# Kernel optimization log

Measured on AMD Instinct MI355X. Metric: run time of the kernel, lower is better.

The kernel has to match this reference:

```python
import jax, jax.numpy as jnp
import numpy as np

B, S, D = 8, 512, 512
H, DK = 64, 8          # 64 heads hardcoded in SelfAttentiveLBLBiLM
WIDTH = 16             # local window width
NL = 2                 # highway layers
N = S + 2 * WIDTH      # padded sequence length


def setup_inputs() -> dict:
    key = jax.random.key(0)
    ks = jax.random.split(key, 12)
    s = 0.02
    return {
        "inputs": jax.random.normal(ks[0], (B, S, D), jnp.float32),
        "left_pad": jax.random.normal(ks[1], (WIDTH, D), jnp.float32) * s,
        "right_pad": jax.random.normal(ks[2], (WIDTH, D), jnp.float32) * s,
        "l_Wqkv": jax.random.normal(ks[3], (3, D, D), jnp.float32) * s,
        "l_bqkv": jnp.zeros((3, D), jnp.float32),
        "l_Wo": jax.random.normal(ks[4], (D, D), jnp.float32) * s,
        "l_bo": jnp.zeros((D,), jnp.float32),
        "r_Wqkv": jax.random.normal(ks[5], (3, D, D), jnp.float32) * s,
        "r_bqkv": jnp.zeros((3, D), jnp.float32),
        "r_Wo": jax.random.normal(ks[6], (D, D), jnp.float32) * s,
        "r_bo": jnp.zeros((D,), jnp.float32),
        "lhw_W": jax.random.normal(ks[7], (NL, 2 * D, D), jnp.float32) * s,
        "lhw_b": jnp.zeros((NL, 2 * D), jnp.float32),
        "rhw_W": jax.random.normal(ks[8], (NL, 2 * D, D), jnp.float32) * s,
        "rhw_b": jnp.zeros((NL, 2 * D), jnp.float32),
    }


def _masks(n, width):
    i = jnp.arange(n)[:, None]
    j = jnp.arange(n)[None, :]
    # local_mask: triu(k=-width-1) * (1 - triu(k=1)) -> i-width-1 <= j <= i
    left = (j <= i) & (j >= i - width - 1)
    # right mask is the full flip of the left mask
    right = (j >= i) & (j <= i + width + 1)
    return left, right


def _mha(x, Wqkv, bqkv, Wo, bo, mask):
    b, n, d = x.shape
    # torch Linear: y = x @ W.T + b, W is [out, in]
    qkv = jnp.einsum("bnd,tod->tbno", x, Wqkv) + bqkv[:, None, None, :]
    q, k, v = [t.reshape(b, n, H, DK).transpose(0, 2, 1, 3) for t in qkv]
    scores = jnp.einsum("bhqd,bhkd->bhqk", q, k) / jnp.sqrt(jnp.float32(DK))
    scores = jnp.where(mask[None, None], scores, jnp.float32(-1e9))
    p = jax.nn.softmax(scores, axis=-1)
    out = jnp.einsum("bhqk,bhkd->bhqd", p, v)
    out = out.transpose(0, 2, 1, 3).reshape(b, n, d)
    return out @ Wo.T + bo


def _highway(x, Ws, bs):
    for l in range(NL):
        proj = x @ Ws[l].T + bs[l]
        nonlin = jax.nn.relu(proj[..., :D])
        gate = jax.nn.sigmoid(proj[..., D:])
        x = gate * x + (1.0 - gate) * nonlin
    return x


def reference(inputs, left_pad, right_pad, l_Wqkv, l_bqkv, l_Wo, l_bo,
              r_Wqkv, r_bqkv, r_Wo, r_bo, lhw_W, lhw_b, rhw_W, rhw_b):
    b = inputs.shape[0]
    new_inputs = jnp.concatenate(
        [jnp.broadcast_to(left_pad[None], (b, WIDTH, D)), inputs,
         jnp.broadcast_to(right_pad[None], (b, WIDTH, D))], axis=1)  # [B, N, D]
    left_mask, right_mask = _masks(N, WIDTH)
    new_left = _mha(new_inputs, l_Wqkv, l_bqkv, l_Wo, l_bo, left_mask)
    new_right = _mha(new_inputs, r_Wqkv, r_bqkv, r_Wo, r_bo, right_mask)
    # per-step loop indexes position start + width -> slice [WIDTH : WIDTH + S]
    left_out = _highway(new_left[:, WIDTH:WIDTH + S], lhw_W, lhw_b)
    right_out = _highway(new_right[:, WIDTH:WIDTH + S], rhw_W, rhw_b)
    last = jnp.concatenate([left_out, right_out], axis=-1)  # [B, S, 2D]
    all_layers = last[None]  # [1, B, S, 2D] (single layer stacked on dim 0)
    return (all_layers, last)
```

## Files before the change

### kernel.cpp

```cpp
#include <hip/hip_runtime.h>
#include <math.h>

#define B_ 8
#define S_ 512
#define D_ 512
#define WIDTH_ 16
#define NSEQ 544
#define MROWS 4352
#define MOUT 4096
#define OUTHALF 4194304

typedef _Float16 half8 __attribute__((ext_vector_type(8)));
typedef _Float16 half4 __attribute__((ext_vector_type(4)));
typedef float floatx4 __attribute__((ext_vector_type(4)));

#define GLD16(g, l) __builtin_amdgcn_global_load_lds(                          \
    (const __attribute__((address_space(1))) void*)(g),                        \
    (__attribute__((address_space(3))) void*)(l), 16, 0, 0)

__device__ __forceinline__ float sigmoidf_(float x) {
    return 1.f / (1.f + __expf(-x));
}

__global__ __launch_bounds__(256)
void gemm_qkv(const _Float16* __restrict__ A,
              const _Float16* __restrict__ B0, const _Float16* __restrict__ B1,
              const float* __restrict__ bias0, const float* __restrict__ bias1,
              _Float16* __restrict__ C16) {
    const int lda = 512, ldb = 512, ldc = 1536, K = 512;
    __shared__ _Float16 As[128 * 32];
    __shared__ _Float16 Bs[128 * 32];
    const int t    = threadIdx.x;
    const int wave = t >> 6;
    const int lane = t & 63;
    const int bm = blockIdx.y * 128;
    const int bn = blockIdx.x * 128;
    const int z  = blockIdx.z;
    const _Float16* B = z ? B1 : B0;
    const float* bias = z ? bias1 : bias0;
    _Float16* C = C16 + (size_t)z * MROWS * 1536;
    const int wm = (wave & 1) * 64;
    const int wn = (wave >> 1) * 64;

    const int inst = wave * 2;
    const int r0 = inst * 16 + (lane >> 2);
    const int kf = (lane & 3) * 8;

    const _Float16* Ag0 = A + (size_t)(bm + r0) * lda + kf;
    const _Float16* Ag1 = Ag0 + (size_t)16 * lda;
    const _Float16* Bg0 = B + (size_t)(bn + r0) * ldb + kf;
    const _Float16* Bg1 = Bg0 + (size_t)16 * ldb;
    _Float16* As0 = &As[inst * 512];
    _Float16* As1 = As0 + 512;
    _Float16* Bs0 = &Bs[inst * 512];
    _Float16* Bs1 = Bs0 + 512;

    const int fr = lane & 15;
    const int fq = (lane >> 4) * 8;

    floatx4 acc[4][4] = {};

    for (int k0 = 0; k0 < K; k0 += 32) {
        GLD16(Ag0, As0); GLD16(Ag1, As1);
        GLD16(Bg0, Bs0); GLD16(Bg1, Bs1);
        Ag0 += 32; Ag1 += 32; Bg0 += 32; Bg1 += 32;
        __syncthreads();
        half8 af[4], bf[4];
#pragma unroll
        for (int s = 0; s < 4; s++) {
            af[s] = *(const half8*)&As[(wm + s * 16 + fr) * 32 + fq];
            bf[s] = *(const half8*)&Bs[(wn + s * 16 + fr) * 32 + fq];
        }
#pragma unroll
        for (int i = 0; i < 4; i++)
#pragma unroll
            for (int j = 0; j < 4; j++)
                acc[i][j] = __builtin_amdgcn_mfma_f32_16x16x32_f16(
                    af[i], bf[j], acc[i][j], 0, 0, 0);
        __syncthreads();
    }

    const int rq = (lane >> 4) * 4;
    const int cc = lane & 15;
#pragma unroll
    for (int i = 0; i < 4; i++) {
        const int rbase = bm + wm + i * 16 + rq;
#pragma unroll
        for (int j = 0; j < 4; j++) {
            const int col = bn + wn + j * 16 + cc;
            const float bv = bias[col];
#pragma unroll
            for (int r = 0; r < 4; r++)
                C[(size_t)(rbase + r) * ldc + col] = (_Float16)(acc[i][j][r] + bv);
        }
    }
}

__global__ __launch_bounds__(256)
void gemm_wo(const _Float16* __restrict__ Aall,
             const _Float16* __restrict__ B0, const _Float16* __restrict__ B1,
             const float* __restrict__ bias0, const float* __restrict__ bias1,
             float* __restrict__ xbase,
             _Float16* __restrict__ x16base) {
    const int lda = 512, ldb = 512, K = 512;
    __shared__ _Float16 As[64 * 32];
    __shared__ _Float16 Bs[128 * 32];
    const int t    = threadIdx.x;
    const int wave = t >> 6;
    const int lane = t & 63;
    const int bm = blockIdx.y * 64;
    const int bn = blockIdx.x * 128;
    const int z  = blockIdx.z;
    const _Float16* A = Aall + (size_t)z * MROWS * 512;
    const _Float16* B = z ? B1 : B0;
    const float* bias = z ? bias1 : bias0;
    float* xcol = xbase + z * 512;
    _Float16* x16 = x16base + (size_t)z * MOUT * 512;

    const int wm = (wave & 1) * 32;
    const int wn = (wave >> 1) * 64;

    const int rA = wave * 16 + (lane >> 2);
    const int rB = wave * 32 + (lane >> 2);
    const int kf = (lane & 3) * 8;

    const _Float16* Ag0 = A + (size_t)(bm + rA) * lda + kf;
    const _Float16* Bg0 = B + (size_t)(bn + rB) * ldb + kf;
    const _Float16* Bg1 = Bg0 + (size_t)16 * ldb;
    _Float16* As0 = &As[wave * 512];
    _Float16* Bs0 = &Bs[wave * 1024];
    _Float16* Bs1 = Bs0 + 512;

    const int fr = lane & 15;
    const int fq = (lane >> 4) * 8;

    floatx4 acc[2][4] = {};

    for (int k0 = 0; k0 < K; k0 += 32) {
        GLD16(Ag0, As0);
        GLD16(Bg0, Bs0); GLD16(Bg1, Bs1);
        Ag0 += 32; Bg0 += 32; Bg1 += 32;
        __syncthreads();
        half8 af[2], bf[4];
#pragma unroll
        for (int s = 0; s < 2; s++)
            af[s] = *(const half8*)&As[(wm + s * 16 + fr) * 32 + fq];
#pragma unroll
        for (int s = 0; s < 4; s++)
            bf[s] = *(const half8*)&Bs[(wn + s * 16 + fr) * 32 + fq];
#pragma unroll
        for (int i = 0; i < 2; i++)
#pragma unroll
            for (int j = 0; j < 4; j++)
                acc[i][j] = __builtin_amdgcn_mfma_f32_16x16x32_f16(
                    af[i], bf[j], acc[i][j], 0, 0, 0);
        __syncthreads();
    }

    const int rq = (lane >> 4) * 4;
    const int cc = lane & 15;
#pragma unroll
    for (int i = 0; i < 2; i++) {
        const int rbase = bm + wm + i * 16 + rq;
#pragma unroll
        for (int r = 0; r < 4; r++) {
            const int row = rbase + r;
            const int b = row / NSEQ;
            const int s = row - b * NSEQ;
            if (s < WIDTH_ || s >= WIDTH_ + S_) continue;
            const int m = b * S_ + s - WIDTH_;
#pragma unroll
            for (int j = 0; j < 4; j++) {
                const int col = bn + wn + j * 16 + cc;
                const float v = acc[i][j][r] + bias[col];
                xcol[(size_t)m * 1024 + col] = v;
                x16[(size_t)m * 512 + col] = (_Float16)v;
            }
        }
    }
}

__global__ __launch_bounds__(256)
void gemm_hw(const _Float16* __restrict__ A16base,
             const _Float16* __restrict__ W0, const _Float16* __restrict__ W1,
             const float* __restrict__ b0, const float* __restrict__ b1,
             float* __restrict__ xbase,
             _Float16* __restrict__ x16outbase,
             float* __restrict__ out2base) {
    const int lda = 512, ldb = 512, K = 512;
    __shared__ _Float16 As[64 * 32];
    __shared__ _Float16 Bn[128 * 32];
    __shared__ _Float16 Bg[128 * 32];
    const int t    = threadIdx.x;
    const int wave = t >> 6;
    const int lane = t & 63;
    const int bm = blockIdx.y * 64;
    const int bn = blockIdx.x * 128;
    const int z  = blockIdx.z;
    const _Float16* A = A16base + (size_t)z * MOUT * 512;
    const _Float16* W = z ? W1 : W0;
    const float* bias = z ? b1 : b0;
    float* xcol = xbase + z * 512;
    _Float16* x16out = x16outbase ? x16outbase + (size_t)z * MOUT * 512 : nullptr;
    float* out2 = out2base ? out2base + z * 512 : nullptr;

    const int wm = (wave & 1) * 32;
    const int wn = (wave >> 1) * 64;

    const int rA = wave * 16 + (lane >> 2);
    const int rB = wave * 32 + (lane >> 2);
    const int kf = (lane & 3) * 8;

    const _Float16* Ag0 = A + (size_t)(bm + rA) * lda + kf;
    const _Float16* Bn0 = W + (size_t)(bn + rB) * ldb + kf;
    const _Float16* Bn1 = Bn0 + (size_t)16 * ldb;
    const _Float16* Bg0 = W + (size_t)(512 + bn + rB) * ldb + kf;
    const _Float16* Bg1 = Bg0 + (size_t)16 * ldb;
    _Float16* As0  = &As[wave * 512];
    _Float16* Bns0 = &Bn[wave * 1024];
    _Float16* Bns1 = Bns0 + 512;
    _Float16* Bgs0 = &Bg[wave * 1024];
    _Float16* Bgs1 = Bgs0 + 512;

    const int fr = lane & 15;
    const int fq = (lane >> 4) * 8;

    floatx4 accn[2][4] = {};
    floatx4 accg[2][4] = {};

    for (int k0 = 0; k0 < K; k0 += 32) {
        GLD16(Ag0, As0);
        GLD16(Bn0, Bns0); GLD16(Bn1, Bns1);
        GLD16(Bg0, Bgs0); GLD16(Bg1, Bgs1);
        Ag0 += 32; Bn0 += 32; Bn1 += 32; Bg0 += 32; Bg1 += 32;
        __syncthreads();
        half8 af[2], bnf[4], bgf[4];
#pragma unroll
        for (int s = 0; s < 2; s++)
            af[s] = *(const half8*)&As[(wm + s * 16 + fr) * 32 + fq];
#pragma unroll
        for (int s = 0; s < 4; s++) {
            bnf[s] = *(const half8*)&Bn[(wn + s * 16 + fr) * 32 + fq];
            bgf[s] = *(const half8*)&Bg[(wn + s * 16 + fr) * 32 + fq];
        }
#pragma unroll
        for (int i = 0; i < 2; i++)
#pragma unroll
            for (int j = 0; j < 4; j++) {
                accn[i][j] = __builtin_amdgcn_mfma_f32_16x16x32_f16(
                    af[i], bnf[j], accn[i][j], 0, 0, 0);
                accg[i][j] = __builtin_amdgcn_mfma_f32_16x16x32_f16(
                    af[i], bgf[j], accg[i][j], 0, 0, 0);
            }
        __syncthreads();
    }

    const int rq = (lane >> 4) * 4;
    const int cc = lane & 15;
#pragma unroll
    for (int i = 0; i < 2; i++) {
        const int rbase = bm + wm + i * 16 + rq;
#pragma unroll
        for (int j = 0; j < 4; j++) {
            const int col = bn + wn + j * 16 + cc;
            const float bnl = bias[col];
            const float bgt = bias[512 + col];
#pragma unroll
            for (int r = 0; r < 4; r++) {
                const int row = rbase + r;
                const float nl = fmaxf(accn[i][j][r] + bnl, 0.f);
                const float g  = sigmoidf_(accg[i][j][r] + bgt);
                const float xo = xcol[(size_t)row * 1024 + col];
                const float v  = g * xo + (1.f - g) * nl;
                xcol[(size_t)row * 1024 + col] = v;
                if (out2)   out2[(size_t)row * 1024 + col] = v;
                if (x16out) x16out[(size_t)row * 512 + col] = (_Float16)v;
            }
        }
    }
}

__global__ __launch_bounds__(256)
void attn_win(const _Float16* __restrict__ qkvall, _Float16* __restrict__ attall) {
    const int dir = blockIdx.y;
    const int dlo = dir ? 0 : -(WIDTH_ + 1);
    const _Float16* qkv = qkvall + (size_t)dir * MROWS * 1536;
    _Float16* att = attall + (size_t)dir * MROWS * 512;
    const int tid = blockIdx.x * 256 + threadIdx.x;
    const int h  = tid & 63;
    const int bi = tid >> 6;
    const int i  = bi % NSEQ;
    const int b  = bi / NSEQ;
    const int j0 = i + dlo;
    const float scale = 0.35355339059327373f;

    const half8 q8 = *(const half8*)(qkv + (size_t)bi * 1536 + h * 8);
    float q[8];
#pragma unroll
    for (int d = 0; d < 8; d++) q[d] = (float)q8[d];

    float s[18];
    float mx = -1e30f;
#pragma unroll
    for (int jj = 0; jj < 18; jj++) {
        const int j = j0 + jj;
        const int jc = j < 0 ? 0 : (j > NSEQ - 1 ? NSEQ - 1 : j);
        const half8 k8 = *(const half8*)(qkv + (size_t)(b * NSEQ + jc) * 1536 + 512 + h * 8);
        float d = 0.f;
#pragma unroll
        for (int dd = 0; dd < 8; dd++) d = fmaf(q[dd], (float)k8[dd], d);
        s[jj] = (j == jc) ? d * scale : -1e30f;
        mx = fmaxf(mx, s[jj]);
    }
    float sum = 0.f;
#pragma unroll
    for (int jj = 0; jj < 18; jj++) { s[jj] = __expf(s[jj] - mx); sum += s[jj]; }
    const float inv = 1.f / sum;

    float o[8] = {};
#pragma unroll
    for (int jj = 0; jj < 18; jj++) {
        const int j = j0 + jj;
        const int jc = j < 0 ? 0 : (j > NSEQ - 1 ? NSEQ - 1 : j);
        const half8 v8 = *(const half8*)(qkv + (size_t)(b * NSEQ + jc) * 1536 + 1024 + h * 8);
        const float p = s[jj];
#pragma unroll
        for (int dd = 0; dd < 8; dd++) o[dd] = fmaf(p, (float)v8[dd], o[dd]);
    }
    half8 o16;
#pragma unroll
    for (int d = 0; d < 8; d++) o16[d] = (_Float16)(o[d] * inv);
    *(half8*)&att[(size_t)bi * 512 + h * 8] = o16;
}

__global__ void cvt_all(const float* __restrict__ lq, const float* __restrict__ rq,
                        const float* __restrict__ lo, const float* __restrict__ ro,
                        const float* __restrict__ lh, const float* __restrict__ rh,
                        _Float16* __restrict__ dst) {
    int idx = blockIdx.x * blockDim.x + threadIdx.x;
    if (idx >= 1048576) return;
    const float* src; int off;
    if      (idx < 196608) { src = lq; off = idx; }
    else if (idx < 393216) { src = rq; off = idx - 196608; }
    else if (idx < 458752) { src = lo; off = idx - 393216; }
    else if (idx < 524288) { src = ro; off = idx - 458752; }
    else if (idx < 786432) { src = lh; off = idx - 524288; }
    else                   { src = rh; off = idx - 786432; }
    const float4 v = ((const float4*)src)[off];
    half4 h = { (_Float16)v.x, (_Float16)v.y, (_Float16)v.z, (_Float16)v.w };
    ((half4*)dst)[idx] = h;
}

__global__ void pad_concat16(const float* __restrict__ inp,
                             const float* __restrict__ lp,
                             const float* __restrict__ rp,
                             _Float16* __restrict__ out) {
    int idx = blockIdx.x * blockDim.x + threadIdx.x;
    if (idx >= MROWS * 128) return;
    const int c4 = idx & 127;
    const int t  = idx >> 7;
    const int n = t % NSEQ;
    const int b = t / NSEQ;
    const float* src;
    if (n < WIDTH_)            src = lp + n * 512;
    else if (n < WIDTH_ + S_)  src = inp + ((size_t)(b * S_ + n - WIDTH_)) * 512;
    else                       src = rp + (n - WIDTH_ - S_) * 512;
    const float4 v = *(const float4*)(src + c4 * 4);
    half4 h = { (_Float16)v.x, (_Float16)v.y, (_Float16)v.z, (_Float16)v.w };
    *(half4*)&out[(size_t)t * 512 + c4 * 4] = h;
}

extern "C" void kernel_launch(void* const* d_in, const int* in_sizes, int n_in,
                              void* d_out, int out_size, void* d_ws, size_t ws_size,
                              hipStream_t stream) {
    const float* inputs    = (const float*)d_in[0];
    const float* left_pad  = (const float*)d_in[1];
    const float* right_pad = (const float*)d_in[2];
    const float* l_Wqkv = (const float*)d_in[3];
    const float* l_bqkv = (const float*)d_in[4];
    const float* l_Wo   = (const float*)d_in[5];
    const float* l_bo   = (const float*)d_in[6];
    const float* r_Wqkv = (const float*)d_in[7];
    const float* r_bqkv = (const float*)d_in[8];
    const float* r_Wo   = (const float*)d_in[9];
    const float* r_bo   = (const float*)d_in[10];
    const float* lhw_W  = (const float*)d_in[11];
    const float* lhw_b  = (const float*)d_in[12];
    const float* rhw_W  = (const float*)d_in[13];
    const float* rhw_b  = (const float*)d_in[14];

    float* out = (float*)d_out;
    _Float16* h = (_Float16*)d_ws;

    _Float16* padX16 = h;
    _Float16* w16    = h + 2228224;
    _Float16* lqkv16 = w16;
    _Float16* rqkv16 = w16 + 786432;
    _Float16* lWo16  = w16 + 1572864;
    _Float16* rWo16  = w16 + 1835008;
    _Float16* lhw16  = w16 + 2097152;
    _Float16* rhw16  = w16 + 3145728;
    _Float16* qkv16  = h + 6422528;
    _Float16* att16  = h + 19791872;
    _Float16* x16a   = h + 24248320;
    _Float16* x16b   = h + 28442624;

    float* out_all  = out;
    float* out_last = out + OUTHALF;

    cvt_all<<<4096, 256, 0, stream>>>(l_Wqkv, r_Wqkv, l_Wo, r_Wo, lhw_W, rhw_W, w16);
    pad_concat16<<<(MROWS * 128 + 255) / 256, 256, 0, stream>>>(
        inputs, left_pad, right_pad, padX16);

    gemm_qkv<<<dim3(12, 34, 2), 256, 0, stream>>>(
        padX16, lqkv16, rqkv16, l_bqkv, r_bqkv, qkv16);

    attn_win<<<dim3(MROWS * 64 / 256, 2), 256, 0, stream>>>(qkv16, att16);

    gemm_wo<<<dim3(4, 68, 2), 256, 0, stream>>>(
        att16, lWo16, rWo16, l_bo, r_bo, out_last, x16a);

    gemm_hw<<<dim3(4, 64, 2), 256, 0, stream>>>(
        x16a, lhw16, rhw16, lhw_b, rhw_b, out_last, x16b, nullptr);
    gemm_hw<<<dim3(4, 64, 2), 256, 0, stream>>>(
        x16b, lhw16 + 524288, rhw16 + 524288, lhw_b + 1024, rhw_b + 1024,
        out_last, nullptr, out_all);
}
```

Before: 229.0 us.

## Drop fp32 residual buffer in highway, retile highway GEMM, merge prep kernels

The highway layers now read the residual input from the fp16 activation buffer instead of keeping an fp32 copy in the output. The Wo GEMM therefore writes only fp16, and the first highway layer writes only fp16 with no fp32 read-modify-write. The highway GEMM tile changes from 64x128 to 128x64 per block, and the weight-conversion and pad-concat kernels are merged into one launch. This cuts global fp32 traffic and one launch, but the residual is now carried in fp16, which adds rounding error.

```diff
diff --git a/kernel.cpp b/kernel.cpp
--- a/kernel.cpp
+++ b/kernel.cpp
@@ -100,7 +100,6 @@
 void gemm_wo(const _Float16* __restrict__ Aall,
              const _Float16* __restrict__ B0, const _Float16* __restrict__ B1,
              const float* __restrict__ bias0, const float* __restrict__ bias1,
-             float* __restrict__ xbase,
              _Float16* __restrict__ x16base) {
     const int lda = 512, ldb = 512, K = 512;
     __shared__ _Float16 As[64 * 32];
@@ -114,7 +113,6 @@
     const _Float16* A = Aall + (size_t)z * MROWS * 512;
     const _Float16* B = z ? B1 : B0;
     const float* bias = z ? bias1 : bias0;
-    float* xcol = xbase + z * 512;
     _Float16* x16 = x16base + (size_t)z * MOUT * 512;
 
     const int wm = (wave & 1) * 32;
@@ -172,81 +170,75 @@
 #pragma unroll
             for (int j = 0; j < 4; j++) {
                 const int col = bn + wn + j * 16 + cc;
-                const float v = acc[i][j][r] + bias[col];
-                xcol[(size_t)m * 1024 + col] = v;
-                x16[(size_t)m * 512 + col] = (_Float16)v;
+                x16[(size_t)m * 512 + col] = (_Float16)(acc[i][j][r] + bias[col]);
             }
         }
     }
 }
 
 __global__ __launch_bounds__(256)
-void gemm_hw(const _Float16* __restrict__ A16base,
+void gemm_hw(const _Float16* __restrict__ x16inbase,
              const _Float16* __restrict__ W0, const _Float16* __restrict__ W1,
              const float* __restrict__ b0, const float* __restrict__ b1,
-             float* __restrict__ xbase,
              _Float16* __restrict__ x16outbase,
-             float* __restrict__ out2base) {
+             float* __restrict__ outlastbase,
+             float* __restrict__ outallbase) {
     const int lda = 512, ldb = 512, K = 512;
-    __shared__ _Float16 As[64 * 32];
-    __shared__ _Float16 Bn[128 * 32];
-    __shared__ _Float16 Bg[128 * 32];
+    __shared__ _Float16 As[128 * 32];
+    __shared__ _Float16 Bn[64 * 32];
+    __shared__ _Float16 Bg[64 * 32];
     const int t    = threadIdx.x;
     const int wave = t >> 6;
     const int lane = t & 63;
-    const int bm = blockIdx.y * 64;
-    const int bn = blockIdx.x * 128;
+    const int bm = blockIdx.y * 128;
+    const int bn = blockIdx.x * 64;
     const int z  = blockIdx.z;
-    const _Float16* A = A16base + (size_t)z * MOUT * 512;
+    const _Float16* A = x16inbase + (size_t)z * MOUT * 512;
     const _Float16* W = z ? W1 : W0;
     const float* bias = z ? b1 : b0;
-    float* xcol = xbase + z * 512;
     _Float16* x16out = x16outbase ? x16outbase + (size_t)z * MOUT * 512 : nullptr;
-    float* out2 = out2base ? out2base + z * 512 : nullptr;
-
-    const int wm = (wave & 1) * 32;
-    const int wn = (wave >> 1) * 64;
-
-    const int rA = wave * 16 + (lane >> 2);
-    const int rB = wave * 32 + (lane >> 2);
+
+    const int wm = (wave & 1) * 64;
+    const int wn = (wave >> 1) * 32;
+
+    const int rA = wave * 32 + (lane >> 2);
+    const int rB = wave * 16 + (lane >> 2);
     const int kf = (lane & 3) * 8;
 
     const _Float16* Ag0 = A + (size_t)(bm + rA) * lda + kf;
+    const _Float16* Ag1 = Ag0 + (size_t)16 * lda;
     const _Float16* Bn0 = W + (size_t)(bn + rB) * ldb + kf;
-    const _Float16* Bn1 = Bn0 + (size_t)16 * ldb;
     const _Float16* Bg0 = W + (size_t)(512 + bn + rB) * ldb + kf;
-    const _Float16* Bg1 = Bg0 + (size_t)16 * ldb;
-    _Float16* As0  = &As[wave * 512];
-    _Float16* Bns0 = &Bn[wave * 1024];
-    _Float16* Bns1 = Bns0 + 512;
-    _Float16* Bgs0 = &Bg[wave * 1024];
-    _Float16* Bgs1 = Bgs0 + 512;
+    _Float16* As0  = &As[wave * 1024];
+    _Float16* As1  = As0 + 512;
+    _Float16* Bns0 = &Bn[wave * 512];
+    _Float16* Bgs0 = &Bg[wave * 512];
 
     const int fr = lane & 15;
     const int fq = (lane >> 4) * 8;
 
-    floatx4 accn[2][4] = {};
-    floatx4 accg[2][4] = {};
+    floatx4 accn[4][2] = {};
+    floatx4 accg[4][2] = {};
 
     for (int k0 = 0; k0 < K; k0 += 32) {
-        GLD16(Ag0, As0);
-        GLD16(Bn0, Bns0); GLD16(Bn1, Bns1);
-        GLD16(Bg0, Bgs0); GLD16(Bg1, Bgs1);
-        Ag0 += 32; Bn0 += 32; Bn1 += 32; Bg0 += 32; Bg1 += 32;
-        __syncthreads();
-        half8 af[2], bnf[4], bgf[4];
-#pragma unroll
-        for (int s = 0; s < 2; s++)
+        GLD16(Ag0, As0); GLD16(Ag1, As1);
+        GLD16(Bn0, Bns0);
+        GLD16(Bg0, Bgs0);
+        Ag0 += 32; Ag1 += 32; Bn0 += 32; Bg0 += 32;
+        __syncthreads();
+        half8 af[4], bnf[2], bgf[2];
+#pragma unroll
+        for (int s = 0; s < 4; s++)
             af[s] = *(const half8*)&As[(wm + s * 16 + fr) * 32 + fq];
 #pragma unroll
-        for (int s = 0; s < 4; s++) {
+        for (int s = 0; s < 2; s++) {
             bnf[s] = *(const half8*)&Bn[(wn + s * 16 + fr) * 32 + fq];
             bgf[s] = *(const half8*)&Bg[(wn + s * 16 + fr) * 32 + fq];
         }
 #pragma unroll
-        for (int i = 0; i < 2; i++)
-#pragma unroll
-            for (int j = 0; j < 4; j++) {
+        for (int i = 0; i < 4; i++)
+#pragma unroll
+            for (int j = 0; j < 2; j++) {
                 accn[i][j] = __builtin_amdgcn_mfma_f32_16x16x32_f16(
                     af[i], bnf[j], accn[i][j], 0, 0, 0);
                 accg[i][j] = __builtin_amdgcn_mfma_f32_16x16x32_f16(
@@ -255,13 +247,16 @@
         __syncthreads();
     }
 
+    float* outlast = outlastbase ? outlastbase + z * 512 : nullptr;
+    float* outall  = outallbase  ? outallbase  + z * 512 : nullptr;
+
     const int rq = (lane >> 4) * 4;
     const int cc = lane & 15;
 #pragma unroll
-    for (int i = 0; i < 2; i++) {
+    for (int i = 0; i < 4; i++) {
         const int rbase = bm + wm + i * 16 + rq;
 #pragma unroll
-        for (int j = 0; j < 4; j++) {
+        for (int j = 0; j < 2; j++) {
             const int col = bn + wn + j * 16 + cc;
             const float bnl = bias[col];
             const float bgt = bias[512 + col];
@@ -270,11 +265,14 @@
                 const int row = rbase + r;
                 const float nl = fmaxf(accn[i][j][r] + bnl, 0.f);
                 const float g  = sigmoidf_(accg[i][j][r] + bgt);
-                const float xo = xcol[(size_t)row * 1024 + col];
+                const float xo = (float)A[(size_t)row * 512 + col];
                 const float v  = g * xo + (1.f - g) * nl;
-                xcol[(size_t)row * 1024 + col] = v;
-                if (out2)   out2[(size_t)row * 1024 + col] = v;
-                if (x16out) x16out[(size_t)row * 512 + col] = (_Float16)v;
+                if (x16out) {
+                    x16out[(size_t)row * 512 + col] = (_Float16)v;
+                } else {
+                    outlast[(size_t)row * 1024 + col] = v;
+                    outall[(size_t)row * 1024 + col] = v;
+                }
             }
         }
     }
@@ -333,41 +331,41 @@
     *(half8*)&att[(size_t)bi * 512 + h * 8] = o16;
 }
 
-__global__ void cvt_all(const float* __restrict__ lq, const float* __restrict__ rq,
-                        const float* __restrict__ lo, const float* __restrict__ ro,
-                        const float* __restrict__ lh, const float* __restrict__ rh,
-                        _Float16* __restrict__ dst) {
-    int idx = blockIdx.x * blockDim.x + threadIdx.x;
-    if (idx >= 1048576) return;
-    const float* src; int off;
-    if      (idx < 196608) { src = lq; off = idx; }
-    else if (idx < 393216) { src = rq; off = idx - 196608; }
-    else if (idx < 458752) { src = lo; off = idx - 393216; }
-    else if (idx < 524288) { src = ro; off = idx - 458752; }
-    else if (idx < 786432) { src = lh; off = idx - 524288; }
-    else                   { src = rh; off = idx - 786432; }
-    const float4 v = ((const float4*)src)[off];
-    half4 h = { (_Float16)v.x, (_Float16)v.y, (_Float16)v.z, (_Float16)v.w };
-    ((half4*)dst)[idx] = h;
-}
-
-__global__ void pad_concat16(const float* __restrict__ inp,
-                             const float* __restrict__ lp,
-                             const float* __restrict__ rp,
-                             _Float16* __restrict__ out) {
-    int idx = blockIdx.x * blockDim.x + threadIdx.x;
-    if (idx >= MROWS * 128) return;
-    const int c4 = idx & 127;
-    const int t  = idx >> 7;
-    const int n = t % NSEQ;
-    const int b = t / NSEQ;
-    const float* src;
-    if (n < WIDTH_)            src = lp + n * 512;
-    else if (n < WIDTH_ + S_)  src = inp + ((size_t)(b * S_ + n - WIDTH_)) * 512;
-    else                       src = rp + (n - WIDTH_ - S_) * 512;
-    const float4 v = *(const float4*)(src + c4 * 4);
-    half4 h = { (_Float16)v.x, (_Float16)v.y, (_Float16)v.z, (_Float16)v.w };
-    *(half4*)&out[(size_t)t * 512 + c4 * 4] = h;
+__global__ void prep(const float* __restrict__ lq, const float* __restrict__ rq,
+                     const float* __restrict__ lo, const float* __restrict__ ro,
+                     const float* __restrict__ lh, const float* __restrict__ rh,
+                     _Float16* __restrict__ wdst,
+                     const float* __restrict__ inp,
+                     const float* __restrict__ lp,
+                     const float* __restrict__ rp,
+                     _Float16* __restrict__ padX) {
+    const int gb = blockIdx.x;
+    if (gb < 4096) {
+        int idx = gb * 256 + threadIdx.x;
+        const float* src; int off;
+        if      (idx < 196608) { src = lq; off = idx; }
+        else if (idx < 393216) { src = rq; off = idx - 196608; }
+        else if (idx < 458752) { src = lo; off = idx - 393216; }
+        else if (idx < 524288) { src = ro; off = idx - 458752; }
+        else if (idx < 786432) { src = lh; off = idx - 524288; }
+        else                   { src = rh; off = idx - 786432; }
+        const float4 v = ((const float4*)src)[off];
+        half4 h = { (_Float16)v.x, (_Float16)v.y, (_Float16)v.z, (_Float16)v.w };
+        ((half4*)wdst)[idx] = h;
+    } else {
+        int idx = (gb - 4096) * 256 + threadIdx.x;
+        const int c4 = idx & 127;
+        const int t  = idx >> 7;
+        const int n = t % NSEQ;
+        const int b = t / NSEQ;
+        const float* src;
+        if (n < WIDTH_)            src = lp + n * 512;
+        else if (n < WIDTH_ + S_)  src = inp + ((size_t)(b * S_ + n - WIDTH_)) * 512;
+        else                       src = rp + (n - WIDTH_ - S_) * 512;
+        const float4 v = *(const float4*)(src + c4 * 4);
+        half4 h = { (_Float16)v.x, (_Float16)v.y, (_Float16)v.z, (_Float16)v.w };
+        *(half4*)&padX[(size_t)t * 512 + c4 * 4] = h;
+    }
 }
 
 extern "C" void kernel_launch(void* const* d_in, const int* in_sizes, int n_in,
@@ -408,9 +406,8 @@
     float* out_all  = out;
     float* out_last = out + OUTHALF;
 
-    cvt_all<<<4096, 256, 0, stream>>>(l_Wqkv, r_Wqkv, l_Wo, r_Wo, lhw_W, rhw_W, w16);
-    pad_concat16<<<(MROWS * 128 + 255) / 256, 256, 0, stream>>>(
-        inputs, left_pad, right_pad, padX16);
+    prep<<<6272, 256, 0, stream>>>(l_Wqkv, r_Wqkv, l_Wo, r_Wo, lhw_W, rhw_W, w16,
+                                   inputs, left_pad, right_pad, padX16);
 
     gemm_qkv<<<dim3(12, 34, 2), 256, 0, stream>>>(
         padX16, lqkv16, rqkv16, l_bqkv, r_bqkv, qkv16);
@@ -418,11 +415,11 @@
     attn_win<<<dim3(MROWS * 64 / 256, 2), 256, 0, stream>>>(qkv16, att16);
 
     gemm_wo<<<dim3(4, 68, 2), 256, 0, stream>>>(
-        att16, lWo16, rWo16, l_bo, r_bo, out_last, x16a);
-
-    gemm_hw<<<dim3(4, 64, 2), 256, 0, stream>>>(
-        x16a, lhw16, rhw16, lhw_b, rhw_b, out_last, x16b, nullptr);
-    gemm_hw<<<dim3(4, 64, 2), 256, 0, stream>>>(
+        att16, lWo16, rWo16, l_bo, r_bo, x16a);
+
+    gemm_hw<<<dim3(8, 32, 2), 256, 0, stream>>>(
+        x16a, lhw16, rhw16, lhw_b, rhw_b, x16b, nullptr, nullptr);
+    gemm_hw<<<dim3(8, 32, 2), 256, 0, stream>>>(
         x16b, lhw16 + 524288, rhw16 + 524288, lhw_b + 1024, rhw_b + 1024,
-        out_last, nullptr, out_all);
-}
+        nullptr, out_last, out_all);
+}
```

After: 220.6 us. 3.7% less time.
